# Optimization experiments

Hardware: AMD Instinct MI355X
Metric: run time of the kernel (lower is better)

Reference implementation:

```python
import jax, jax.numpy as jnp
import numpy as np

B, C, H, W = 16, 512, 64, 64
L, D = 77, 768
NH = 8
HD = C // NH
EPS = 1e-5


def layernorm(x, g, b):
    m = jnp.mean(x, axis=-1, keepdims=True)
    v = jnp.var(x, axis=-1, keepdims=True)
    return (x - m) * jax.lax.rsqrt(v + EPS) * g + b


def setup_inputs() -> dict:
    key = jax.random.key(0)
    ks = jax.random.split(key, 12)
    s_c = 1.0 / np.sqrt(C)
    s_d = 1.0 / np.sqrt(D)
    return {
        "x": jax.random.normal(ks[0], (B, C, H, W), jnp.float32),
        "text_features": jax.random.normal(ks[1], (B, L, D), jnp.float32),
        "wq": jax.random.normal(ks[2], (C, C), jnp.float32) * s_c,
        "bq": jnp.zeros((C,), jnp.float32),
        "wk": jax.random.normal(ks[3], (C, D), jnp.float32) * s_d,
        "bk": jnp.zeros((C,), jnp.float32),
        "wv": jax.random.normal(ks[4], (C, D), jnp.float32) * s_d,
        "bv": jnp.zeros((C,), jnp.float32),
        "wo": jax.random.normal(ks[5], (C, C), jnp.float32) * s_c,
        "bo": jnp.zeros((C,), jnp.float32),
        "g1": jnp.ones((C,), jnp.float32),
        "b1": jnp.zeros((C,), jnp.float32),
        "g2": jnp.ones((C,), jnp.float32),
        "b2": jnp.zeros((C,), jnp.float32),
    }


def reference(x, text_features, wq, bq, wk, bk, wv, bv, wo, bo, g1, b1, g2, b2):
    b, c, h, w = x.shape
    # 1x1 conv query projection
    q = jnp.einsum('bchw,oc->bohw', x, wq) + bq[None, :, None, None]
    # 2D positional encoding: first c/2 channels vary along w, next c/2 along h
    pos_x = jnp.broadcast_to(jnp.linspace(0.0, 1.0, w)[None, :], (h, w))
    pos_y = jnp.broadcast_to(jnp.linspace(0.0, 1.0, h)[:, None], (h, w))
    pe = jnp.concatenate([
        jnp.broadcast_to(pos_x[None], (c // 2, h, w)),
        jnp.broadcast_to(pos_y[None], (c // 2, h, w)),
    ], axis=0)  # [C,H,W]
    q = q + 0.05 * pe[None]
    # flatten spatial -> tokens, layernorm over channels
    q_flat = q.reshape(b, c, h * w).transpose(0, 2, 1)  # [B,HW,C]
    q_norm = layernorm(q_flat, g1, b1)
    qh = q_norm.reshape(b, h * w, NH, HD)  # [B,HW,NH,HD]
    # text key/value projections
    k = jnp.einsum('bld,cd->blc', text_features, wk) + bk
    v = jnp.einsum('bld,cd->blc', text_features, wv) + bv
    k_norm = layernorm(k, g2, b2)
    kh = k_norm.reshape(b, -1, NH, HD)
    vh = v.reshape(b, -1, NH, HD)
    scale = HD ** -0.5
    attn = jnp.einsum('bqhd,bkhd->bhqk', qh, kh) * scale  # [B,NH,HW,L]
    attn = jax.nn.softmax(attn, axis=-1)  # dropout is identity in eval
    out = jnp.einsum('bhqk,bkhd->bqhd', attn, vh).reshape(b, h * w, c)
    out = out.transpose(0, 2, 1).reshape(b, c, h, w)
    out = jnp.einsum('bchw,oc->bohw', out, wo) + bo[None, :, None, None]
    return out + x
```

## Files before the change

kernel.cpp:

```cpp
#include <hip/hip_runtime.h>
#include <stdint.h>

#define BD   16
#define CD   512
#define HD_  64
#define NH_  8
#define HWD  4096
#define LD   77
#define DD   768

typedef __bf16 bf16;
typedef bf16 bf16x8 __attribute__((ext_vector_type(8)));
typedef float f32x4 __attribute__((ext_vector_type(4)));

__device__ __forceinline__ void async16(const bf16* g, bf16* l) {
  __builtin_amdgcn_global_load_lds(
      (const __attribute__((address_space(1))) void*)g,
      (__attribute__((address_space(3))) void*)l, 16, 0, 0);
}

__device__ __forceinline__ unsigned short bfb(float f) {
  bf16 h = (bf16)f;
  return __builtin_bit_cast(unsigned short, h);
}

__global__ __launch_bounds__(256) void xpose_cvt(const float* __restrict__ X,
                                                 bf16* __restrict__ Y) {
  __shared__ float tile[64][68];
  const int b = blockIdx.z, c0 = blockIdx.y * 64, t0 = blockIdx.x * 64;
  const int tid = threadIdx.x;
  const float* Xb = X + ((size_t)b * CD + c0) * HWD + t0;
#pragma unroll
  for (int p = 0; p < 4; ++p) {
    int c = (tid >> 4) + p * 16;
    int t = (tid & 15) * 4;
    float4 v = *(const float4*)(Xb + (size_t)c * HWD + t);
    *(float4*)&tile[c][t] = v;
  }
  __syncthreads();
  int t = tid >> 2, cb = (tid & 3) * 16;
  union { uint4 u[2]; unsigned short us[16]; } pk;
#pragma unroll
  for (int j = 0; j < 16; ++j) pk.us[j] = bfb(tile[cb + j][t]);
  uint4* Yp = (uint4*)(Y + ((size_t)(b * HWD + t0 + t)) * CD + c0 + cb);
  Yp[0] = pk.u[0];
  Yp[1] = pk.u[1];
}

__global__ __launch_bounds__(256) void cvt_all(
    const float* __restrict__ t, const float* __restrict__ q,
    const float* __restrict__ k, const float* __restrict__ v,
    const float* __restrict__ o, bf16* __restrict__ tb, bf16* __restrict__ qb,
    bf16* __restrict__ kb, bf16* __restrict__ vb, bf16* __restrict__ ob) {
  int bid = blockIdx.x;
  const float* src;
  bf16* dst;
  if (bid < 462) { src = t; dst = tb; }
  else if (bid < 590) { src = q; dst = qb; bid -= 462; }
  else if (bid < 782) { src = k; dst = kb; bid -= 590; }
  else if (bid < 974) { src = v; dst = vb; bid -= 782; }
  else { src = o; dst = ob; bid -= 974; }
  int i = (bid * 256 + threadIdx.x) * 8;
  float4 a = *(const float4*)(src + i);
  float4 c = *(const float4*)(src + i + 4);
  union { uint4 u; unsigned short us[8]; } pk;
  pk.us[0] = bfb(a.x); pk.us[1] = bfb(a.y); pk.us[2] = bfb(a.z); pk.us[3] = bfb(a.w);
  pk.us[4] = bfb(c.x); pk.us[5] = bfb(c.y); pk.us[6] = bfb(c.z); pk.us[7] = bfb(c.w);
  *(uint4*)(dst + i) = pk.u;
}

template <int TM, int TN, int MODE, int NBX>
__global__ __launch_bounds__(256)
void gemm_bt(const bf16* __restrict__ A, const bf16* __restrict__ B,
             int M, int N, int K,
             const float* __restrict__ bias, const float* __restrict__ xres,
             float* __restrict__ D,
             const bf16* __restrict__ B2, const float* __restrict__ bias2,
             float* __restrict__ D2) {
  constexpr int WM = TM / 2, WN = TN / 2;
  constexpr int AFR = WM / 16, BFR = WN / 16;
  constexpr int ACH = TM / 8, TCH = (TM + TN) / 8, WCH = TCH / 4;
  __shared__ bf16 sA[TM * 64];
  __shared__ bf16 sB[TN * 64];
  const int tid = threadIdx.x, wave = tid >> 6, lane = tid & 63;
  int flat = blockIdx.x;
  {
    const int qq = (int)gridDim.x >> 3;
    flat = (flat & 7) * qq + (flat >> 3);
  }
  const int m0 = (flat / NBX) * TM;
  int n0 = (flat % NBX) * TN;
  if constexpr (MODE == 2) {
    if (n0 >= (N >> 1)) { B = B2; bias = bias2; D = D2; n0 -= (N >> 1); }
  }
  const int wm = (wave >> 1) * WM, wn = (wave & 1) * WN;
  const int sub = lane >> 3, col8 = (lane & 7) * 8;
  const int mlo = lane & 15, khi = lane >> 4;
  f32x4 acc[AFR][BFR] = {};

  for (int k0 = 0; k0 < K; k0 += 64) {
#pragma unroll
    for (int r = 0; r < WCH; ++r) {
      int ci = wave * WCH + r;
      if (ci < ACH) {
        int row = ci * 8 + sub;
        int g = m0 + row;
        if (g > M - 1) g = M - 1;
        async16(A + (size_t)g * K + k0 + col8, &sA[ci * 512]);
      } else {
        int cj = ci - ACH;
        int row = cj * 8 + sub;
        async16(B + (size_t)(n0 + row) * K + k0 + col8, &sB[cj * 512]);
      }
    }
    __syncthreads();
#pragma unroll
    for (int kc = 0; kc < 2; ++kc) {
      bf16x8 af[AFR], bfv[BFR];
      const int ko = kc * 32 + khi * 8;
#pragma unroll
      for (int i = 0; i < AFR; ++i)
        af[i] = *(const bf16x8*)&sA[(wm + i * 16 + mlo) * 64 + ko];
#pragma unroll
      for (int j = 0; j < BFR; ++j)
        bfv[j] = *(const bf16x8*)&sB[(wn + j * 16 + mlo) * 64 + ko];
#pragma unroll
      for (int i = 0; i < AFR; ++i)
#pragma unroll
        for (int j = 0; j < BFR; ++j)
          acc[i][j] = __builtin_amdgcn_mfma_f32_16x16x32_bf16(af[i], bfv[j],
                                                              acc[i][j], 0, 0, 0);
    }
    __syncthreads();
  }

  if constexpr (MODE == 0) {
    __shared__ float sRS[TM][2][2];
    bf16* Dq = (bf16*)D;
    const int wnh = wave & 1;
#pragma unroll
    for (int i = 0; i < AFR; ++i) {
#pragma unroll
      for (int r = 0; r < 4; ++r) {
        const int rowt = wm + i * 16 + khi * 4 + r;
        const int m = m0 + rowt;
        const int hw = m & (HWD - 1);
        const float pex = (float)(hw & 63) * (0.05f / 63.0f);
        const float pey = (float)(hw >> 6) * (0.05f / 63.0f);
        float s = 0.f, sq = 0.f;
#pragma unroll
        for (int j = 0; j < BFR; ++j) {
          const int n = n0 + wn + j * 16 + mlo;
          float v = acc[i][j][r] + bias[n] + (n < 256 ? pex : pey);
          bf16 hv = (bf16)v;
          Dq[(size_t)m * CD + n] = hv;
          float vr = (float)hv;
          s += vr;
          sq += vr * vr;
        }
        s += __shfl_xor(s, 1); sq += __shfl_xor(sq, 1);
        s += __shfl_xor(s, 2); sq += __shfl_xor(sq, 2);
        s += __shfl_xor(s, 4); sq += __shfl_xor(sq, 4);
        s += __shfl_xor(s, 8); sq += __shfl_xor(sq, 8);
        if (mlo == 0) { sRS[rowt][wnh][0] = s; sRS[rowt][wnh][1] = sq; }
      }
    }
    __syncthreads();
    if (tid < TM) {
      float s = sRS[tid][0][0] + sRS[tid][1][0];
      float sq = sRS[tid][0][1] + sRS[tid][1][1];
      float2* pst = (float2*)xres;
      pst[(size_t)(n0 >> 7) * (BD * HWD) + (m0 + tid)] = make_float2(s, sq);
    }
  } else if constexpr (MODE == 3) {
    float bn[BFR];
#pragma unroll
    for (int j = 0; j < BFR; ++j) bn[j] = bias[n0 + wn + j * 16 + mlo];
#pragma unroll
    for (int i = 0; i < AFR; ++i) {
      const int m = m0 + wm + i * 16 + khi * 4;
      const int b = m >> 12, hw = m & (HWD - 1);
      const float* xr0 = xres + ((size_t)b * CD) * HWD + hw;
      float* d0 = D + ((size_t)b * CD) * HWD + hw;
#pragma unroll
      for (int j = 0; j < BFR; ++j) {
        const size_t off = (size_t)(n0 + wn + j * 16 + mlo) * HWD;
        float4 xr = *(const float4*)(xr0 + off);
        float4 ov;
        ov.x = acc[i][j][0] + bn[j] + xr.x;
        ov.y = acc[i][j][1] + bn[j] + xr.y;
        ov.z = acc[i][j][2] + bn[j] + xr.z;
        ov.w = acc[i][j][3] + bn[j] + xr.w;
        *(float4*)(d0 + off) = ov;
      }
    }
  } else {
#pragma unroll
    for (int i = 0; i < AFR; ++i) {
      const int mb = m0 + wm + i * 16 + khi * 4;
#pragma unroll
      for (int j = 0; j < BFR; ++j) {
        const int n = n0 + wn + j * 16 + mlo;
#pragma unroll
        for (int r = 0; r < 4; ++r) {
          const int m = mb + r;
          if (m < M) D[(size_t)m * CD + n] = acc[i][j][r] + bias[n];
        }
      }
    }
  }
}

__global__ __launch_bounds__(256) void ln_rows(const float* __restrict__ X,
                                               const float* __restrict__ gg,
                                               const float* __restrict__ bb,
                                               bf16* __restrict__ Y, int nrows,
                                               int khlayout) {
  const int wv = threadIdx.x >> 6, lane = threadIdx.x & 63;
  const int row = blockIdx.x * 4 + wv;
  if (row >= nrows) return;
  const float* xr = X + (size_t)row * CD + lane * 8;
  float4 v0 = *(const float4*)xr;
  float4 v1 = *(const float4*)(xr + 4);
  float xv[8] = {v0.x, v0.y, v0.z, v0.w, v1.x, v1.y, v1.z, v1.w};
  float s = 0.f, sq = 0.f;
#pragma unroll
  for (int j = 0; j < 8; ++j) { s += xv[j]; sq += xv[j] * xv[j]; }
#pragma unroll
  for (int off = 1; off < 64; off <<= 1) {
    s += __shfl_xor(s, off);
    sq += __shfl_xor(sq, off);
  }
  float mean = s * (1.0f / 512.0f);
  float var = sq * (1.0f / 512.0f) - mean * mean;
  float rstd = rsqrtf(var + 1e-5f);
  const int c0 = lane * 8;
  union { uint4 u; unsigned short us[8]; } pk;
#pragma unroll
  for (int j = 0; j < 8; ++j)
    pk.us[j] = bfb((xv[j] - mean) * rstd * gg[c0 + j] + bb[c0 + j]);
  size_t ya;
  if (khlayout) {
    int bq = row / LD, l = row - bq * LD;
    int hh = lane >> 3, dd = (lane & 7) * 8;
    ya = (((size_t)(bq * NH_ + hh)) * LD + l) * HD_ + dd;
  } else {
    ya = (size_t)row * CD + c0;
  }
  *(uint4*)(Y + ya) = pk.u;
}

__global__ __launch_bounds__(256) void make_vt(const float* __restrict__ vraw,
                                               bf16* __restrict__ vt) {
  const int bh = blockIdx.x, b = bh >> 3, h = bh & 7;
  const int tid = threadIdx.x, d = tid & 63, lg = tid >> 6;
  for (int l = lg; l < 96; l += 4) {
    float v = 0.f;
    if (l < LD) v = vraw[((size_t)(b * LD + l)) * CD + h * HD_ + d];
    vt[((size_t)(bh * HD_ + d)) * 96 + l] = (bf16)v;
  }
}

__global__ __launch_bounds__(256) void attn_k(const bf16* __restrict__ Q,
                                              const float2* __restrict__ PST,
                                              const float* __restrict__ G1,
                                              const float* __restrict__ B1,
                                              const bf16* __restrict__ KH,
                                              const bf16* __restrict__ VT,
                                              bf16* __restrict__ O) {
  __shared__ bf16 P[4][16 * 104];
  const int tid = threadIdx.x, wv = tid >> 6, lane = tid & 63;
  const int m = lane & 15, kg = lane >> 4;
  const int q0 = blockIdx.x * 64, h = blockIdx.y, b = blockIdx.z;
  const int bh = b * NH_ + h;

  const int rowg = b * HWD + q0 + wv * 16 + m;
  const size_t qoff = (size_t)rowg * CD + h * HD_;
  bf16x8 a0r = *(const bf16x8*)(Q + qoff + kg * 8);
  bf16x8 a1r = *(const bf16x8*)(Q + qoff + 32 + kg * 8);

  float2 st = PST[(size_t)kg * (BD * HWD) + rowg];
  float s = st.x, sq = st.y;
  s += __shfl_xor(s, 16); sq += __shfl_xor(sq, 16);
  s += __shfl_xor(s, 32); sq += __shfl_xor(sq, 32);
  const float mean = s * (1.0f / 512.0f);
  const float var = sq * (1.0f / 512.0f) - mean * mean;
  const float rstd = rsqrtf(var + 1e-5f);

  const int c0 = h * HD_ + kg * 8;
  float4 ga = *(const float4*)(G1 + c0), gb = *(const float4*)(G1 + c0 + 4);
  float4 gc = *(const float4*)(G1 + c0 + 32), gd = *(const float4*)(G1 + c0 + 36);
  float4 ta = *(const float4*)(B1 + c0), tb = *(const float4*)(B1 + c0 + 4);
  float4 tc = *(const float4*)(B1 + c0 + 32), td = *(const float4*)(B1 + c0 + 36);
  const float gg[16] = {ga.x, ga.y, ga.z, ga.w, gb.x, gb.y, gb.z, gb.w,
                        gc.x, gc.y, gc.z, gc.w, gd.x, gd.y, gd.z, gd.w};
  const float bbv[16] = {ta.x, ta.y, ta.z, ta.w, tb.x, tb.y, tb.z, tb.w,
                         tc.x, tc.y, tc.z, tc.w, td.x, td.y, td.z, td.w};
  bf16x8 a0, a1;
#pragma unroll
  for (int e = 0; e < 8; ++e) {
    a0[e] = (bf16)(((float)a0r[e] - mean) * rstd * gg[e] + bbv[e]);
    a1[e] = (bf16)(((float)a1r[e] - mean) * rstd * gg[8 + e] + bbv[8 + e]);
  }

  const bf16* Kb = KH + (size_t)bh * LD * HD_;
  f32x4 sacc[5];
#pragma unroll
  for (int kt = 0; kt < 5; ++kt) {
    int key = kt * 16 + m;
    if (key > LD - 1) key = LD - 1;
    const bf16* kr = Kb + key * HD_ + kg * 8;
    bf16x8 b0 = *(const bf16x8*)kr;
    bf16x8 b1 = *(const bf16x8*)(kr + 32);
    f32x4 z = {0.f, 0.f, 0.f, 0.f};
    z = __builtin_amdgcn_mfma_f32_16x16x32_bf16(a0, b0, z, 0, 0, 0);
    z = __builtin_amdgcn_mfma_f32_16x16x32_bf16(a1, b1, z, 0, 0, 0);
    sacc[kt] = z;
  }

  bf16* Pw = &P[wv][0];
#pragma unroll
  for (int r = 0; r < 4; ++r) {
    float sc[5];
#pragma unroll
    for (int kt = 0; kt < 5; ++kt) {
      float v = sacc[kt][r] * 0.125f;
      if (kt == 4 && m >= LD - 64) v = -3.0e38f;
      sc[kt] = v;
    }
    float mx = fmaxf(fmaxf(fmaxf(sc[0], sc[1]), fmaxf(sc[2], sc[3])), sc[4]);
    mx = fmaxf(mx, __shfl_xor(mx, 1));
    mx = fmaxf(mx, __shfl_xor(mx, 2));
    mx = fmaxf(mx, __shfl_xor(mx, 4));
    mx = fmaxf(mx, __shfl_xor(mx, 8));
    float sum = 0.f;
#pragma unroll
    for (int kt = 0; kt < 5; ++kt) {
      sc[kt] = __expf(sc[kt] - mx);
      sum += sc[kt];
    }
    sum += __shfl_xor(sum, 1);
    sum += __shfl_xor(sum, 2);
    sum += __shfl_xor(sum, 4);
    sum += __shfl_xor(sum, 8);
    float inv = 1.0f / sum;
    const int prow = kg * 4 + r;
#pragma unroll
    for (int kt = 0; kt < 5; ++kt)
      Pw[prow * 104 + kt * 16 + m] = (bf16)(sc[kt] * inv);
    Pw[prow * 104 + 80 + m] = (bf16)0.f;
  }
  __syncthreads();

  bf16x8 ap[3];
#pragma unroll
  for (int kc = 0; kc < 3; ++kc)
    ap[kc] = *(const bf16x8*)&Pw[m * 104 + kc * 32 + kg * 8];

  const bf16* Vb = VT + (size_t)bh * HD_ * 96;
  f32x4 o[4] = {};
#pragma unroll
  for (int nt = 0; nt < 4; ++nt) {
#pragma unroll
    for (int kc = 0; kc < 3; ++kc) {
      bf16x8 bv = *(const bf16x8*)(Vb + (nt * 16 + m) * 96 + kc * 32 + kg * 8);
      o[nt] = __builtin_amdgcn_mfma_f32_16x16x32_bf16(ap[kc], bv, o[nt], 0, 0, 0);
    }
  }
#pragma unroll
  for (int nt = 0; nt < 4; ++nt)
#pragma unroll
    for (int r = 0; r < 4; ++r) {
      const int row = b * HWD + q0 + wv * 16 + kg * 4 + r;
      O[(size_t)row * CD + h * HD_ + nt * 16 + m] = (bf16)(o[nt][r]);
    }
}

extern "C" void kernel_launch(void* const* d_in, const int* in_sizes, int n_in,
                              void* d_out, int out_size, void* d_ws, size_t ws_size,
                              hipStream_t stream) {
  const float* x    = (const float*)d_in[0];
  const float* text = (const float*)d_in[1];
  const float* wq   = (const float*)d_in[2];
  const float* bq   = (const float*)d_in[3];
  const float* wk   = (const float*)d_in[4];
  const float* bk   = (const float*)d_in[5];
  const float* wv   = (const float*)d_in[6];
  const float* bv   = (const float*)d_in[7];
  const float* wo   = (const float*)d_in[8];
  const float* bo   = (const float*)d_in[9];
  const float* g1   = (const float*)d_in[10];
  const float* b1   = (const float*)d_in[11];
  const float* g2   = (const float*)d_in[12];
  const float* b2   = (const float*)d_in[13];
  float* out = (float*)d_out;

  char* p = (char*)d_ws;
  auto alloc = [&](size_t bytes) {
    char* r = p;
    p += (bytes + 255) & ~(size_t)255;
    return r;
  };
  bf16* xt     = (bf16*)alloc((size_t)BD * HWD * CD * 2);
  bf16* attn_o = (bf16*)alloc((size_t)BD * HWD * CD * 2);
  bf16* textb  = (bf16*)alloc((size_t)BD * LD * DD * 2);
  bf16* wqb    = (bf16*)alloc((size_t)CD * CD * 2);
  bf16* wkb    = (bf16*)alloc((size_t)CD * DD * 2);
  bf16* wvb    = (bf16*)alloc((size_t)CD * DD * 2);
  bf16* wob    = (bf16*)alloc((size_t)CD * CD * 2);
  float* kraw  = (float*)alloc((size_t)BD * LD * CD * 4);
  float* vraw  = (float*)alloc((size_t)BD * LD * CD * 4);
  bf16* kh     = (bf16*)alloc((size_t)BD * NH_ * LD * HD_ * 2);
  bf16* vt     = (bf16*)alloc((size_t)BD * NH_ * HD_ * 96 * 2);
  float* pstat = (float*)alloc((size_t)4 * BD * HWD * 2 * 4);
  bf16* qbf = (bf16*)out;

  xpose_cvt<<<dim3(HWD / 64, CD / 64, BD), 256, 0, stream>>>(x, xt);
  cvt_all<<<1102, 256, 0, stream>>>(text, wq, wk, wv, wo,
                                    textb, wqb, wkb, wvb, wob);

  gemm_bt<128, 128, 2, 8><<<80, 256, 0, stream>>>(
      textb, wkb, BD * LD, 2 * CD, DD, bk, nullptr, kraw, wvb, bv, vraw);
  ln_rows<<<(BD * LD + 3) / 4, 256, 0, stream>>>(kraw, g2, b2, kh, BD * LD, 1);
  make_vt<<<BD * NH_, 256, 0, stream>>>(vraw, vt);

  gemm_bt<128, 128, 0, 4><<<2048, 256, 0, stream>>>(
      xt, wqb, BD * HWD, CD, CD, bq, pstat, (float*)qbf,
      nullptr, nullptr, nullptr);

  attn_k<<<dim3(HWD / 64, NH_, BD), 256, 0, stream>>>(
      qbf, (const float2*)pstat, g1, b1, kh, vt, attn_o);

  gemm_bt<128, 128, 3, 4><<<2048, 256, 0, stream>>>(
      attn_o, wob, BD * HWD, CD, CD, bo, x, out, nullptr, nullptr, nullptr);
}
```

Baseline: 557.6 us.

## Double-buffer LDS tiles in bf16 GEMM with async prefetch two tiles ahead

Turns the single-buffered shared-memory staging of the GEMM into a double-buffered pipeline. The next K tile's global-to-LDS async loads are issued before the current tile is consumed, using explicit vmcnt waits and barriers. This is meant to hide global load latency behind the MFMA work. In exchange it doubles the LDS footprint, which may lower occupancy, and it depends on a hardcoded per-wave load count guarded by a static_assert.

Measured after the change: 539.5 us. 3.2% less time.

```diff
diff --git a/kernel.cpp b/kernel.cpp
--- a/kernel.cpp
+++ b/kernel.cpp
@@ -80,8 +80,9 @@
   constexpr int WM = TM / 2, WN = TN / 2;
   constexpr int AFR = WM / 16, BFR = WN / 16;
   constexpr int ACH = TM / 8, TCH = (TM + TN) / 8, WCH = TCH / 4;
-  __shared__ bf16 sA[TM * 64];
-  __shared__ bf16 sB[TN * 64];
+  static_assert(WCH == 8, "vmcnt(8) literal assumes 8 loads/wave/tile");
+  __shared__ bf16 sA[2][TM * 64];
+  __shared__ bf16 sB[2][TN * 64];
   const int tid = threadIdx.x, wave = tid >> 6, lane = tid & 63;
   int flat = blockIdx.x;
   {
@@ -98,7 +99,7 @@
   const int mlo = lane & 15, khi = lane >> 4;
   f32x4 acc[AFR][BFR] = {};
 
-  for (int k0 = 0; k0 < K; k0 += 64) {
+  auto stage = [&](int buf, int k0) {
 #pragma unroll
     for (int r = 0; r < WCH; ++r) {
       int ci = wave * WCH + r;
@@ -106,24 +107,34 @@
         int row = ci * 8 + sub;
         int g = m0 + row;
         if (g > M - 1) g = M - 1;
-        async16(A + (size_t)g * K + k0 + col8, &sA[ci * 512]);
+        async16(A + (size_t)g * K + k0 + col8, &sA[buf][ci * 512]);
       } else {
         int cj = ci - ACH;
         int row = cj * 8 + sub;
-        async16(B + (size_t)(n0 + row) * K + k0 + col8, &sB[cj * 512]);
+        async16(B + (size_t)(n0 + row) * K + k0 + col8, &sB[buf][cj * 512]);
       }
     }
-    __syncthreads();
+  };
+
+  const int NT = K >> 6;
+  stage(0, 0);
+  stage(1, 64);
+  asm volatile("s_waitcnt vmcnt(8)" ::: "memory");
+  __builtin_amdgcn_s_barrier();
+  __builtin_amdgcn_sched_barrier(0);
+
+  for (int t = 0; t < NT; ++t) {
+    const int cur = t & 1;
 #pragma unroll
     for (int kc = 0; kc < 2; ++kc) {
       bf16x8 af[AFR], bfv[BFR];
       const int ko = kc * 32 + khi * 8;
 #pragma unroll
       for (int i = 0; i < AFR; ++i)
-        af[i] = *(const bf16x8*)&sA[(wm + i * 16 + mlo) * 64 + ko];
+        af[i] = *(const bf16x8*)&sA[cur][(wm + i * 16 + mlo) * 64 + ko];
 #pragma unroll
       for (int j = 0; j < BFR; ++j)
-        bfv[j] = *(const bf16x8*)&sB[(wn + j * 16 + mlo) * 64 + ko];
+        bfv[j] = *(const bf16x8*)&sB[cur][(wn + j * 16 + mlo) * 64 + ko];
 #pragma unroll
       for (int i = 0; i < AFR; ++i)
 #pragma unroll
@@ -131,7 +142,18 @@
           acc[i][j] = __builtin_amdgcn_mfma_f32_16x16x32_bf16(af[i], bfv[j],
                                                               acc[i][j], 0, 0, 0);
     }
-    __syncthreads();
+    asm volatile("s_waitcnt lgkmcnt(0)" ::: "memory");
+    __builtin_amdgcn_s_barrier();
+    if (t + 2 < NT) {
+      stage(cur, (t + 2) << 6);
+      asm volatile("s_waitcnt vmcnt(8)" ::: "memory");
+      __builtin_amdgcn_s_barrier();
+      __builtin_amdgcn_sched_barrier(0);
+    } else if (t + 1 < NT) {
+      asm volatile("s_waitcnt vmcnt(0)" ::: "memory");
+      __builtin_amdgcn_s_barrier();
+      __builtin_amdgcn_sched_barrier(0);
+    }
   }
 
   if constexpr (MODE == 0) {
```
